# Kernel optimization log

Measured on AMD Instinct MI355X. Metric: run time of the kernel, lower is better.

The kernel has to match this reference:

```python
import jax, jax.numpy as jnp
import numpy as np

EPS = 1e-5  # GroupNorm eps (torch default)


def _groupnorm1(x, w, b):
    # x: [N, C]; GroupNorm(1, C) on [N, C, 1, 1] -> normalize over all C per sample
    mu = jnp.mean(x, axis=1, keepdims=True)
    var = jnp.mean(jnp.square(x - mu), axis=1, keepdims=True)
    xn = (x - mu) * jax.lax.rsqrt(var + EPS)
    return xn * w[None, :] + b[None, :]


def setup_inputs() -> dict:
    key = jax.random.key(0)
    ks = jax.random.split(key, 4)
    C, R = 512, 8
    Cr = C // R
    x = jax.random.normal(ks[0], (32, C, 56, 56), dtype=jnp.float32)
    # kaiming-ish scaled init for 1x1 convs
    w1 = jax.random.normal(ks[1], (Cr, C), dtype=jnp.float32) * (1.0 / np.sqrt(C))
    b1 = jnp.zeros((Cr,), dtype=jnp.float32)
    gn1_w = jnp.ones((Cr,), dtype=jnp.float32)
    gn1_b = jnp.zeros((Cr,), dtype=jnp.float32)
    w2 = jax.random.normal(ks[2], (C, Cr), dtype=jnp.float32) * (1.0 / np.sqrt(Cr))
    b2 = jnp.zeros((C,), dtype=jnp.float32)
    gn2_w = jnp.ones((C,), dtype=jnp.float32)
    gn2_b = jnp.zeros((C,), dtype=jnp.float32)
    return {"x": x, "w1": w1, "b1": b1, "gn1_w": gn1_w, "gn1_b": gn1_b,
            "w2": w2, "b2": b2, "gn2_w": gn2_w, "gn2_b": gn2_b}


def reference(x, w1, b1, gn1_w, gn1_b, w2, b2, gn2_w, gn2_b):
    # Global average pool: [N, C, H, W] -> [N, C]
    pooled = jnp.mean(x, axis=(2, 3))
    # 1x1 conv == matmul on channels
    h = jnp.einsum('nc,rc->nr', pooled, w1) + b1[None, :]
    h = _groupnorm1(h, gn1_w, gn1_b)
    h = jax.nn.elu(h)  # alpha=1.0, torch default
    g = jnp.einsum('nr,cr->nc', h, w2) + b2[None, :]
    g = _groupnorm1(g, gn2_w, gn2_b)
    gate = jax.nn.sigmoid(g)
    # Broadcast channel gate over spatial dims
    return x * gate[:, :, None, None]
```

## Files before the change

### kernel.cpp

```cpp
#include <hip/hip_runtime.h>
#include <math.h>

#define N_ 32
#define C_ 512
#define CR_ 64
#define HW_ 3136
#define HW4_ 784
#define HROWS_ 8192
constexpr float EPS = 1e-5f;

typedef float f4 __attribute__((ext_vector_type(4)));

__device__ __forceinline__ void pool_row(const float* __restrict__ x,
                                         float* __restrict__ pooled, int row) {
    const f4* xr = reinterpret_cast<const f4*>(x + (size_t)row * HW_);
    float acc = 0.f;
    for (int j = threadIdx.x; j < HW4_; j += 256) {
        f4 v = xr[j];
        acc += (v.x + v.y) + (v.z + v.w);
    }
    for (int o = 32; o; o >>= 1) acc += __shfl_down(acc, o, 64);
    __shared__ float s[4];
    if ((threadIdx.x & 63) == 0) s[threadIdx.x >> 6] = acc;
    __syncthreads();
    if (threadIdx.x == 0)
        pooled[row] = (s[0] + s[1] + s[2] + s[3]) * (1.0f / HW_);
}

__device__ __forceinline__ void scale_row(const float* __restrict__ x,
                                          const float* __restrict__ gate,
                                          float* __restrict__ out, int row) {
    const float g = gate[row];
    const f4* xr = reinterpret_cast<const f4*>(x + (size_t)row * HW_);
    f4* orow = reinterpret_cast<f4*>(out + (size_t)row * HW_);
    for (int j = threadIdx.x; j < HW4_; j += 256) {
        f4 v = xr[j];
        v *= g;
        __builtin_nontemporal_store(v, &orow[j]);
    }
}

__device__ __forceinline__ void gate_sample(
    const float* __restrict__ pooled,
    const float* __restrict__ w1, const float* __restrict__ b1,
    const float* __restrict__ gw1, const float* __restrict__ gb1,
    const float* __restrict__ w2, const float* __restrict__ b2,
    const float* __restrict__ gw2, const float* __restrict__ gb2,
    float* __restrict__ gate, int n)
{
    const int tid = threadIdx.x;
    __shared__ float sp[C_];
    __shared__ float sh[CR_];
    __shared__ float sred[4];
    const int base = n * C_;
    sp[tid]       = pooled[base + tid];
    sp[tid + 256] = pooled[base + 256 + tid];
    __syncthreads();

    {
        const int r = tid >> 2, l4 = tid & 3;
        float a = 0.f;
        for (int cc = l4; cc < C_; cc += 4) a += sp[cc] * w1[r * C_ + cc];
        a += __shfl_xor(a, 1, 64);
        a += __shfl_xor(a, 2, 64);
        if (l4 == 0) sh[r] = a + b1[r];
    }
    __syncthreads();

    if (tid < 64) {
        const float v = sh[tid];
        float s = v;
        for (int o = 32; o; o >>= 1) s += __shfl_xor(s, o, 64);
        const float mu = s * (1.0f / CR_);
        const float d = v - mu;
        float vv = d * d;
        for (int o = 32; o; o >>= 1) vv += __shfl_xor(vv, o, 64);
        float xn = d * rsqrtf(vv * (1.0f / CR_) + EPS) * gw1[tid] + gb1[tid];
        sh[tid] = xn > 0.f ? xn : expm1f(xn);
    }
    __syncthreads();

    float g0 = b2[tid], g1 = b2[tid + 256];
    #pragma unroll 8
    for (int r = 0; r < CR_; ++r) {
        g0 += sh[r] * w2[tid * CR_ + r];
        g1 += sh[r] * w2[(tid + 256) * CR_ + r];
    }
    float s = g0 + g1;
    for (int o = 32; o; o >>= 1) s += __shfl_xor(s, o, 64);
    if ((tid & 63) == 0) sred[tid >> 6] = s;
    __syncthreads();
    const float mu = (sred[0] + sred[1] + sred[2] + sred[3]) * (1.0f / C_);
    const float d0 = g0 - mu, d1 = g1 - mu;
    float vv = d0 * d0 + d1 * d1;
    for (int o = 32; o; o >>= 1) vv += __shfl_xor(vv, o, 64);
    __syncthreads();
    if ((tid & 63) == 0) sred[tid >> 6] = vv;
    __syncthreads();
    const float rstd = rsqrtf((sred[0] + sred[1] + sred[2] + sred[3]) * (1.0f / C_) + EPS);
    const float xn0 = d0 * rstd * gw2[tid] + gb2[tid];
    const float xn1 = d1 * rstd * gw2[tid + 256] + gb2[tid + 256];
    gate[base + tid]       = 1.f / (1.f + expf(-xn0));
    gate[base + tid + 256] = 1.f / (1.f + expf(-xn1));
}

__global__ __launch_bounds__(256) void step_kernel(
    const float* __restrict__ x,
    float* __restrict__ pooled, float* __restrict__ gate,
    const float* __restrict__ w1, const float* __restrict__ b1,
    const float* __restrict__ gw1, const float* __restrict__ gb1,
    const float* __restrict__ w2, const float* __restrict__ b2,
    const float* __restrict__ gw2, const float* __restrict__ gb2,
    float* __restrict__ out,
    int nGate, int gateBase, int mode, int rowBase)
{
    const int bid = blockIdx.x;
    if (bid < nGate) {
        gate_sample(pooled, w1, b1, gw1, gb1, w2, b2, gw2, gb2,
                    gate, gateBase + bid);
    } else {
        const int row = rowBase + (bid - nGate);
        if (mode == 0) pool_row(x, pooled, row);
        else           scale_row(x, gate, out, row);
    }
}

extern "C" void kernel_launch(void* const* d_in, const int* in_sizes, int n_in,
                              void* d_out, int out_size, void* d_ws, size_t ws_size,
                              hipStream_t stream) {
    const float* x   = (const float*)d_in[0];
    const float* w1  = (const float*)d_in[1];
    const float* b1  = (const float*)d_in[2];
    const float* gw1 = (const float*)d_in[3];
    const float* gb1 = (const float*)d_in[4];
    const float* w2  = (const float*)d_in[5];
    const float* b2  = (const float*)d_in[6];
    const float* gw2 = (const float*)d_in[7];
    const float* gb2 = (const float*)d_in[8];
    float* out = (float*)d_out;

    float* pooled = (float*)d_ws;
    float* gate   = pooled + N_ * C_;

    #define LAUNCH(grid, nG, gB, md, rB) \
        step_kernel<<<(grid), 256, 0, stream>>>(x, pooled, gate, w1, b1, gw1, gb1, \
                                                w2, b2, gw2, gb2, out, (nG), (gB), (md), (rB))

    LAUNCH(HROWS_, 0, 0, 0, 0);
    LAUNCH(16 + HROWS_, 16, 0, 0, HROWS_);
    LAUNCH(16 + HROWS_, 16, 16, 1, 0);
    LAUNCH(HROWS_, 0, 0, 1, HROWS_);
    #undef LAUNCH
}
```

Measured before the change: 128.7 us.

## Fuse pooling and gate computation via last-block atomic counter per sample

Replaces the four staggered half-batch launches with a pooling kernel in which the last block to finish each sample, detected through an atomic per-sample counter, computes that sample's gate. A separate scale kernel follows. This removes inter-launch overhead and the extra gate-only blocks, at the cost of a memset, atomics, and losing the previous overlap where one half's pooling ran alongside the other half's scaling. The second pass over x may also get less L2 reuse than the half-split schedule gave.

```diff
diff --git a/kernel.cpp b/kernel.cpp
--- a/kernel.cpp
+++ b/kernel.cpp
@@ -6,55 +6,56 @@
 #define CR_ 64
 #define HW_ 3136
 #define HW4_ 784
-#define HROWS_ 8192
 constexpr float EPS = 1e-5f;
 
 typedef float f4 __attribute__((ext_vector_type(4)));
 
-__device__ __forceinline__ void pool_row(const float* __restrict__ x,
-                                         float* __restrict__ pooled, int row) {
-    const f4* xr = reinterpret_cast<const f4*>(x + (size_t)row * HW_);
-    float acc = 0.f;
-    for (int j = threadIdx.x; j < HW4_; j += 256) {
-        f4 v = xr[j];
-        acc += (v.x + v.y) + (v.z + v.w);
-    }
-    for (int o = 32; o; o >>= 1) acc += __shfl_down(acc, o, 64);
-    __shared__ float s[4];
-    if ((threadIdx.x & 63) == 0) s[threadIdx.x >> 6] = acc;
-    __syncthreads();
-    if (threadIdx.x == 0)
-        pooled[row] = (s[0] + s[1] + s[2] + s[3]) * (1.0f / HW_);
-}
+#define LD_A(p)   __hip_atomic_load((p), __ATOMIC_RELAXED, __HIP_MEMORY_SCOPE_AGENT)
+#define ST_A(p,v) __hip_atomic_store((p), (v), __ATOMIC_RELAXED, __HIP_MEMORY_SCOPE_AGENT)
 
-__device__ __forceinline__ void scale_row(const float* __restrict__ x,
-                                          const float* __restrict__ gate,
-                                          float* __restrict__ out, int row) {
-    const float g = gate[row];
-    const f4* xr = reinterpret_cast<const f4*>(x + (size_t)row * HW_);
-    f4* orow = reinterpret_cast<f4*>(out + (size_t)row * HW_);
-    for (int j = threadIdx.x; j < HW4_; j += 256) {
-        f4 v = xr[j];
-        v *= g;
-        __builtin_nontemporal_store(v, &orow[j]);
-    }
-}
-
-__device__ __forceinline__ void gate_sample(
-    const float* __restrict__ pooled,
+__global__ __launch_bounds__(256) void poolgate_kernel(
+    const float* __restrict__ x,
     const float* __restrict__ w1, const float* __restrict__ b1,
     const float* __restrict__ gw1, const float* __restrict__ gb1,
     const float* __restrict__ w2, const float* __restrict__ b2,
     const float* __restrict__ gw2, const float* __restrict__ gb2,
-    float* __restrict__ gate, int n)
+    float* __restrict__ pooled, float* __restrict__ gate,
+    int* __restrict__ cnt)
 {
+    const int row = blockIdx.x;
+    const int n = row >> 9;
     const int tid = threadIdx.x;
+
+    {
+        const f4* xr = reinterpret_cast<const f4*>(x + (size_t)row * HW_);
+        float acc = 0.f;
+        for (int j = tid; j < HW4_; j += 256) {
+            f4 v = xr[j];
+            acc += (v.x + v.y) + (v.z + v.w);
+        }
+        for (int o = 32; o; o >>= 1) acc += __shfl_down(acc, o, 64);
+        __shared__ float s[4];
+        if ((tid & 63) == 0) s[tid >> 6] = acc;
+        __syncthreads();
+        if (tid == 0)
+            ST_A(&pooled[row], (s[0] + s[1] + s[2] + s[3]) * (1.0f / HW_));
+    }
+
+    __shared__ int lastFlag;
+    if (tid == 0) {
+        const int old = __hip_atomic_fetch_add(&cnt[n * 32], 1, __ATOMIC_ACQ_REL,
+                                               __HIP_MEMORY_SCOPE_AGENT);
+        lastFlag = (old == C_ - 1);
+    }
+    __syncthreads();
+    if (!lastFlag) return;
+
     __shared__ float sp[C_];
     __shared__ float sh[CR_];
     __shared__ float sred[4];
     const int base = n * C_;
-    sp[tid]       = pooled[base + tid];
-    sp[tid + 256] = pooled[base + 256 + tid];
+    sp[tid]       = LD_A(&pooled[base + tid]);
+    sp[tid + 256] = LD_A(&pooled[base + 256 + tid]);
     __syncthreads();
 
     {
@@ -104,24 +105,17 @@
     gate[base + tid + 256] = 1.f / (1.f + expf(-xn1));
 }
 
-__global__ __launch_bounds__(256) void step_kernel(
-    const float* __restrict__ x,
-    float* __restrict__ pooled, float* __restrict__ gate,
-    const float* __restrict__ w1, const float* __restrict__ b1,
-    const float* __restrict__ gw1, const float* __restrict__ gb1,
-    const float* __restrict__ w2, const float* __restrict__ b2,
-    const float* __restrict__ gw2, const float* __restrict__ gb2,
-    float* __restrict__ out,
-    int nGate, int gateBase, int mode, int rowBase)
-{
-    const int bid = blockIdx.x;
-    if (bid < nGate) {
-        gate_sample(pooled, w1, b1, gw1, gb1, w2, b2, gw2, gb2,
-                    gate, gateBase + bid);
-    } else {
-        const int row = rowBase + (bid - nGate);
-        if (mode == 0) pool_row(x, pooled, row);
-        else           scale_row(x, gate, out, row);
+__global__ __launch_bounds__(256) void scale_kernel(const float* __restrict__ x,
+                                                    const float* __restrict__ gate,
+                                                    float* __restrict__ out) {
+    const int row = blockIdx.x;
+    const float g = gate[row];
+    const f4* xr = reinterpret_cast<const f4*>(x + (size_t)row * HW_);
+    f4* orow = reinterpret_cast<f4*>(out + (size_t)row * HW_);
+    for (int j = threadIdx.x; j < HW4_; j += 256) {
+        f4 v = xr[j];
+        v *= g;
+        __builtin_nontemporal_store(v, &orow[j]);
     }
 }
 
@@ -141,14 +135,12 @@
 
     float* pooled = (float*)d_ws;
     float* gate   = pooled + N_ * C_;
+    int*   cnt    = (int*)(gate + N_ * C_);
 
-    #define LAUNCH(grid, nG, gB, md, rB) \
-        step_kernel<<<(grid), 256, 0, stream>>>(x, pooled, gate, w1, b1, gw1, gb1, \
-                                                w2, b2, gw2, gb2, out, (nG), (gB), (md), (rB))
+    hipMemsetAsync(cnt, 0, N_ * 32 * sizeof(int), stream);
 
-    LAUNCH(HROWS_, 0, 0, 0, 0);
-    LAUNCH(16 + HROWS_, 16, 0, 0, HROWS_);
-    LAUNCH(16 + HROWS_, 16, 16, 1, 0);
-    LAUNCH(HROWS_, 0, 0, 1, HROWS_);
-    #undef LAUNCH
+    poolgate_kernel<<<N_ * C_, 256, 0, stream>>>(x, w1, b1, gw1, gb1,
+                                                 w2, b2, gw2, gb2,
+                                                 pooled, gate, cnt);
+    scale_kernel<<<N_ * C_, 256, 0, stream>>>(x, gate, out);
 }
```

After: 514.0 us. 299% more time.
